# Performance work log

Hardware: AMD Instinct MI355X
Metric: run time of the kernel (lower is better)

The kernel has to match this reference:

```python
import jax, jax.numpy as jnp
import numpy as np

G = 5   # grid intervals
K = 3   # spline order
D_MODEL, D_FF = 512, 2048
B, S = 2, 2048

def make_grid():
    h = 2.0 / G
    # extended knot vector: G + 2K + 1 points spanning [-1 - K*h, 1 + K*h]
    return (jnp.arange(-K, G + K + 1, dtype=jnp.float32) * h - 1.0)

def b_splines(x, grid, k):
    # x: (N, in), grid: (G+2k+1,) -> bases: (N, in, G+k) via Cox-de Boor
    x = x[..., None]  # (N, in, 1)
    bases = ((x >= grid[:-1]) & (x < grid[1:])).astype(x.dtype)  # order-0, (N,in,G+2k)
    for j in range(1, k + 1):
        left = (x - grid[: -(j + 1)]) / (grid[j:-1] - grid[: -(j + 1)])
        right = (grid[j + 1:] - x) / (grid[j + 1:] - grid[1:-j])
        bases = left * bases[..., :-1] + right * bases[..., 1:]
    return bases

def kan_layer(x, grid, w_base, w_spline):
    # x: (N, in); w_base: (out, in); w_spline: (out, in, G+k)
    base = jax.nn.silu(x) @ w_base.T                      # residual base path
    bases = b_splines(x, grid, K)                          # (N, in, G+k)
    spline = jnp.einsum('nig,oig->no', bases, w_spline)    # per-edge spline contraction
    return base + spline

def setup_inputs() -> dict:
    key = jax.random.key(0)
    ks = jax.random.split(key, 5)
    sc1 = 1.0 / np.sqrt(D_MODEL)
    sc2 = 1.0 / np.sqrt(D_FF)
    return {
        'x': jax.random.normal(ks[0], (B, S, D_MODEL), dtype=jnp.float32),
        'grid': make_grid(),
        'w1_base': jax.random.normal(ks[1], (D_FF, D_MODEL), dtype=jnp.float32) * sc1,
        'w1_spline': jax.random.normal(ks[2], (D_FF, D_MODEL, G + K), dtype=jnp.float32) * (0.1 * sc1),
        'w2_base': jax.random.normal(ks[3], (D_MODEL, D_FF), dtype=jnp.float32) * sc2,
        'w2_spline': jax.random.normal(ks[4], (D_MODEL, D_FF, G + K), dtype=jnp.float32) * (0.1 * sc2),
    }

def reference(x, grid, w1_base, w1_spline, w2_base, w2_spline):
    b, s, d = x.shape
    xf = x.reshape(-1, d)                      # (N, d_model)
    h = kan_layer(xf, grid, w1_base, w1_spline)   # (N, d_ff)
    out = kan_layer(h, grid, w2_base, w2_spline)  # (N, d_model)
    return out.reshape(b, s, d)
```

## Files before the change

kernel.cpp:

```cpp
#include <hip/hip_runtime.h>
#include <stdint.h>


typedef __bf16 bf16x8_t __attribute__((ext_vector_type(8)));
typedef float f32x4_t __attribute__((ext_vector_type(4)));

__device__ __forceinline__ float bf2f(unsigned short u) {
    union { float f; uint32_t i; } c; c.i = ((uint32_t)u) << 16; return c.f;
}
__device__ __forceinline__ unsigned short f2bf(float f) {
    union { float f; uint32_t u; } c; c.f = f;
    uint32_t u = c.u;
    u += 0x7FFFu + ((u >> 16) & 1u);
    return (unsigned short)(u >> 16);
}
__device__ __forceinline__ bool f32world(const void* gridp) {
    return ((*(const unsigned int*)gridp) & 0xFFFFu) == 0xCCCDu;
}

__global__ __launch_bounds__(256)
void cvt4_kernel(const void* __restrict__ s0, const void* __restrict__ s1,
                 const void* __restrict__ s2, const void* __restrict__ s3,
                 unsigned short* __restrict__ dst, const void* __restrict__ gridp)
{
    const int n0 = 262144;
    const int n01 = n0 + 2097152;
    const int n012 = n01 + 262144;
    const int n = n012 + 2097152;
    int i = blockIdx.x * 256 + threadIdx.x;
    if (i >= n) return;
    const void* src; long off;
    if      (i < n0)   { src = s0; off = i; }
    else if (i < n01)  { src = s1; off = i - n0; }
    else if (i < n012) { src = s2; off = i - n01; }
    else               { src = s3; off = i - n012; }
    if (f32world(gridp)) {
        float4 v = ((const float4*)src)[off];
        ushort4 o;
        o.x = f2bf(v.x); o.y = f2bf(v.y); o.z = f2bf(v.z); o.w = f2bf(v.w);
        ((ushort4*)dst)[i] = o;
    } else {
        ((ushort4*)dst)[i] = ((const ushort4*)src)[off];
    }
}

template<int XMODE>
__global__ __launch_bounds__(256)
void act_kernel(const void* __restrict__ Xv, const void* __restrict__ gridp,
                unsigned short* __restrict__ S, unsigned short* __restrict__ BS,
                int total4)
{
    int gi = blockIdx.x * 256 + threadIdx.x;
    if (gi >= total4) return;

    const bool w32 = f32world(gridp);

    float t[12];
    if (w32) {
        const float* g = (const float*)gridp;
#pragma unroll
        for (int k = 0; k < 12; ++k) t[k] = g[k];
    } else {
        const unsigned short* g = (const unsigned short*)gridp;
#pragma unroll
        for (int k = 0; k < 12; ++k) t[k] = bf2f(g[k]);
    }
    const float rr[3] = {1.0f / (t[1] - t[0]), 1.0f / (t[2] - t[0]),
                         1.0f / (t[3] - t[0])};

    float xv[4];
    if (XMODE == 2 || (XMODE == 0 && w32)) {
        float4 v = ((const float4*)Xv)[gi];
        xv[0] = v.x; xv[1] = v.y; xv[2] = v.z; xv[3] = v.w;
    } else {
        ushort4 v = ((const ushort4*)Xv)[gi];
        xv[0] = bf2f(v.x); xv[1] = bf2f(v.y); xv[2] = bf2f(v.z); xv[3] = bf2f(v.w);
    }

    ushort4 sOut;
    unsigned short* sp = (unsigned short*)&sOut;
    int4 bsOut[4];

#pragma unroll
    for (int e = 0; e < 4; ++e) {
        float x = xv[e];
        float sg = 1.0f / (1.0f + __expf(-x));
        sp[e] = f2bf(x * sg);

        float b[11];
#pragma unroll
        for (int j = 0; j < 11; ++j)
            b[j] = (x >= t[j] && x < t[j + 1]) ? 1.0f : 0.0f;

#pragma unroll
        for (int j = 1; j <= 3; ++j) {
            float inv = rr[j - 1];
#pragma unroll
            for (int i = 0; i + j < 11; ++i) {
                float left  = (x - t[i]) * inv;
                float right = (t[i + j + 1] - x) * inv;
                b[i] = left * b[i] + right * b[i + 1];
            }
        }

        union { int4 v; unsigned short h[8]; } u;
#pragma unroll
        for (int g = 0; g < 8; ++g) u.h[g] = f2bf(b[g]);
        bsOut[e] = u.v;
    }

    ((ushort4*)S)[gi] = sOut;
    int4* bp = (int4*)&BS[(long)gi * 32];
#pragma unroll
    for (int e = 0; e < 4; ++e) bp[e] = bsOut[e];
}

template<int BM, int BN, int OUT_MODE>
__global__ __launch_bounds__(256)
void gemm_seg(const unsigned short* __restrict__ A0, int K0,
              const unsigned short* __restrict__ A1, int K1,
              const unsigned short* __restrict__ B0,
              const unsigned short* __restrict__ B1,
              void* __restrict__ Cv, int N, int crow0, int ktiles,
              const void* __restrict__ gridp)
{
    constexpr int BK = 64;
    constexpr int TM = BM / 32;
    constexpr int TN = BN / 32;

    __shared__ unsigned short As[BM * BK];
    __shared__ unsigned short Bs[BN * BK];

    const int tid  = threadIdx.x;
    const int lane = tid & 63;
    const int w    = tid >> 6;
    const int wm   = w & 1;
    const int wn   = w >> 1;

    const int gx = gridDim.x, gy = gridDim.y, gz = gridDim.z;
    int bx = blockIdx.x, by = blockIdx.y, bz = blockIdx.z;
    {
        int NB = gx * gy * gz;
        if ((NB & 7) == 0) {
            int F = bx + gx * (by + gy * bz);
            int T = (F & 7) * (NB >> 3) + (F >> 3);
            int pl = gx * gy;
            bz = T / pl;
            int r = T - bz * pl;
            by = r / gx;
            bx = r - by * gx;
        }
    }

    const int rowA0 = by * BM;
    const int colC0 = bx * BN;

    const int nkt0 = K0 / BK;
    const int nkt  = nkt0 + K1 / BK;
    const int kt0  = bz * ktiles;
    const int kt1  = (kt0 + ktiles < nkt) ? kt0 + ktiles : nkt;

    const int srow = (w << 3) + (lane >> 3);
    const int scol = (((lane & 7) ^ ((lane >> 3) & 7)) << 3);

    const int q  = lane >> 4;
    const int l7 = lane & 7;
    const int cidx0 = ((q) ^ l7) << 3;
    const int cidx1 = ((4 + q) ^ l7) << 3;

    f32x4_t acc[TM][TN];
#pragma unroll
    for (int i = 0; i < TM; ++i)
#pragma unroll
        for (int j = 0; j < TN; ++j)
            acc[i][j] = (f32x4_t){0.f, 0.f, 0.f, 0.f};

    for (int kt = kt0; kt < kt1; ++kt) {
        const unsigned short* Abase;
        const unsigned short* Bbase;
        long ld; int ko;
        if (kt < nkt0) { Abase = A0; Bbase = B0; ld = K0; ko = kt * BK; }
        else           { Abase = A1; Bbase = B1; ld = K1; ko = (kt - nkt0) * BK; }

#pragma unroll
        for (int i = 0; i < BM / 32; ++i) {
            const unsigned short* g = Abase + (long)(rowA0 + i * 32 + srow) * ld + ko + scol;
            __builtin_amdgcn_global_load_lds(
                (const __attribute__((address_space(1))) void*)g,
                (__attribute__((address_space(3))) void*)&As[(i * 32 + (w << 3)) * BK],
                16, 0, 0);
        }
#pragma unroll
        for (int i = 0; i < BN / 32; ++i) {
            const unsigned short* g = Bbase + (long)(colC0 + i * 32 + srow) * ld + ko + scol;
            __builtin_amdgcn_global_load_lds(
                (const __attribute__((address_space(1))) void*)g,
                (__attribute__((address_space(3))) void*)&Bs[(i * 32 + (w << 3)) * BK],
                16, 0, 0);
        }
        __syncthreads();

#pragma unroll
        for (int ks = 0; ks < 2; ++ks) {
            const int cidx = ks ? cidx1 : cidx0;
            bf16x8_t af[TM], bfr[TN];
#pragma unroll
            for (int tm = 0; tm < TM; ++tm)
                af[tm] = *(const bf16x8_t*)&As[(wm * (BM / 2) + tm * 16 + (lane & 15)) * BK
                                               + cidx];
#pragma unroll
            for (int tn = 0; tn < TN; ++tn)
                bfr[tn] = *(const bf16x8_t*)&Bs[(wn * (BN / 2) + tn * 16 + (lane & 15)) * BK
                                                + cidx];
#pragma unroll
            for (int tm = 0; tm < TM; ++tm)
#pragma unroll
                for (int tn = 0; tn < TN; ++tn)
                    acc[tm][tn] = __builtin_amdgcn_mfma_f32_16x16x32_bf16(
                        af[tm], bfr[tn], acc[tm][tn], 0, 0, 0);
        }
        __syncthreads();
    }

    const bool w32 = (OUT_MODE == 2) ? f32world(gridp) : false;
#pragma unroll
    for (int tm = 0; tm < TM; ++tm) {
#pragma unroll
        for (int tn = 0; tn < TN; ++tn) {
            int row0 = crow0 + rowA0 + wm * (BM / 2) + tm * 16 + (lane >> 4) * 4;
            int col  = colC0 + wn * (BN / 2) + tn * 16 + (lane & 15);
#pragma unroll
            for (int r = 0; r < 4; ++r) {
                long off = (long)(row0 + r) * N + col;
                float v = acc[tm][tn][r];
                if (OUT_MODE == 1)      unsafeAtomicAdd(&((float*)Cv)[off], v);
                else if (OUT_MODE == 0) ((unsigned short*)Cv)[off] = f2bf(v);
                else if (w32)           ((float*)Cv)[off] = v;
                else                    ((unsigned short*)Cv)[off] = f2bf(v);
            }
        }
    }
}

__global__ __launch_bounds__(256)
void accum_to_out(const float* __restrict__ acc, void* __restrict__ out,
                  int n4, const void* __restrict__ gridp)
{
    int i = blockIdx.x * 256 + threadIdx.x;
    if (i >= n4) return;
    float4 v = ((const float4*)acc)[i];
    if (f32world(gridp)) {
        ((float4*)out)[i] = v;
    } else {
        ushort4 o;
        o.x = f2bf(v.x); o.y = f2bf(v.y); o.z = f2bf(v.z); o.w = f2bf(v.w);
        ((ushort4*)out)[i] = o;
    }
}

extern "C" void kernel_launch(void* const* d_in, const int* in_sizes, int n_in,
                              void* d_out, int out_size, void* d_ws, size_t ws_size,
                              hipStream_t stream)
{
    const void* x   = d_in[0];
    const void* grd = d_in[1];
    const void* w1b = d_in[2];
    const void* w1s = d_in[3];
    const void* w2b = d_in[4];
    const void* w2s = d_in[5];

    const int NTOK = 4096, D1 = 512, D2 = 2048;
    const size_t MiB = 1024 * 1024;
    char* ws = (char*)d_ws;

    if (ws_size >= 144 * MiB) {
        unsigned short* wcat   = (unsigned short*)ws;
        unsigned short* w1b_bf = (unsigned short*)(ws);
        unsigned short* w1s_bf = (unsigned short*)(ws + 2  * MiB);
        unsigned short* w2b_bf = (unsigned short*)(ws + 18 * MiB);
        unsigned short* w2s_bf = (unsigned short*)(ws + 20 * MiB);
        unsigned short* S1     = (unsigned short*)(ws + 36 * MiB);
        unsigned short* BS1    = (unsigned short*)(ws + 40 * MiB);
        unsigned short* H      = (unsigned short*)(ws + 72 * MiB);
        unsigned short* S2     = (unsigned short*)(ws + 88 * MiB);
        float*          C2     = (float*)(ws + 104 * MiB);
        unsigned short* BS2    = (unsigned short*)(ws + 112 * MiB);

        int CT;
        if      (ws_size >= 240 * MiB) CT = 4096;
        else if (ws_size >= 176 * MiB) CT = 2048;
        else                           CT = 1024;

        cvt4_kernel<<<(4718592 + 255) / 256, 256, 0, stream>>>(w1b, w1s, w2b, w2s, wcat, grd);

        act_kernel<0><<<(NTOK * D1 / 4 + 255) / 256, 256, 0, stream>>>(
            x, grd, S1, BS1, NTOK * D1 / 4);
        {
            dim3 g(D2 / 128, NTOK / 128, 1);
            gemm_seg<128, 128, 0><<<g, 256, 0, stream>>>(
                S1, D1, BS1, D1 * 8, w1b_bf, w1s_bf, (void*)H, D2, 0, 72, grd);
        }

        hipMemsetAsync(C2, 0, (size_t)NTOK * D1 * 4, stream);
        const int SPLIT2 = 32768 / CT;
        const int KT2 = 288 / SPLIT2;
        int nch = NTOK / CT;
        for (int c = 0; c < nch; ++c) {
            long tokOff = (long)c * CT;
            act_kernel<1><<<(CT * D2 / 4 + 255) / 256, 256, 0, stream>>>(
                (const void*)(H + tokOff * D2), grd, S2, BS2, CT * D2 / 4);
            dim3 g(D1 / 128, CT / 128, SPLIT2);
            gemm_seg<128, 128, 1><<<g, 256, 0, stream>>>(
                S2, D2, BS2, D2 * 8, w2b_bf, w2s_bf,
                (void*)C2, D1, (int)tokOff, KT2, grd);
        }

        accum_to_out<<<(NTOK * D1 / 4 + 255) / 256, 256, 0, stream>>>(
            C2, d_out, NTOK * D1 / 4, grd);
    } else {
        unsigned short* w1b_bf = (unsigned short*)(ws);
        unsigned short* w1s_bf = (unsigned short*)(ws + 2  * MiB);
        unsigned short* w2b_bf = (unsigned short*)(ws + 18 * MiB);
        unsigned short* w2s_bf = (unsigned short*)(ws + 20 * MiB);
        unsigned short* H      = (unsigned short*)(ws + 36 * MiB);
        unsigned short* S1     = (unsigned short*)(ws + 52 * MiB);
        unsigned short* BS1    = (unsigned short*)(ws + 56 * MiB);
        unsigned short* S2     = (unsigned short*)(ws + 52 * MiB);
        unsigned short* BS2    = (unsigned short*)(ws + 68 * MiB);

        int CT;
        if      (ws_size >= 100 * MiB) CT = 1024;
        else                           CT = 256;

        cvt4_kernel<<<(4718592 + 255) / 256, 256, 0, stream>>>(
            w1b, w1s, w2b, w2s, (unsigned short*)ws, grd);

        {
            act_kernel<0><<<(NTOK * D1 / 4 + 255) / 256, 256, 0, stream>>>(
                x, grd, S1, BS1, NTOK * D1 / 4);
            dim3 g(D2 / 128, NTOK / 128, 1);
            gemm_seg<128, 128, 0><<<g, 256, 0, stream>>>(
                S1, D1, BS1, D1 * 8, w1b_bf, w1s_bf, (void*)H, D2, 0, 72, grd);
        }
        int nch = NTOK / CT;
        for (int c = 0; c < nch; ++c) {
            long tokOff = (long)c * CT;
            act_kernel<1><<<(CT * D2 / 4 + 255) / 256, 256, 0, stream>>>(
                (const void*)(H + tokOff * D2), grd, S2 + tokOff * D2, BS2, CT * D2 / 4);
            dim3 g(D1 / 128, CT / 64, 1);
            gemm_seg<64, 128, 2><<<g, 256, 0, stream>>>(
                S2 + tokOff * D2, D2, BS2, D2 * 8, w2b_bf, w2s_bf,
                d_out, D1, (int)tokOff, 288, grd);
        }
    }
}
```

Baseline: 393.6 us.

## Split-K the first KAN GEMM into two partial buffers and fold memset into activation

The first-layer GEMM now runs with two K-splits along grid z. Each split writes its own bf16 partial H buffer at an offset of zstride, which roughly doubles the block count for that GEMM. The second-layer activation kernel adds a mode that reads both partials and sums them before computing SiLU and the B-spline bases. The separate memset of the fp32 accumulator is folded into the first activation chunk. In exchange, H traffic roughly doubles, each partial is rounded to bf16 before the sum, and the fast path now needs a larger workspace threshold.

```diff
diff --git a/kernel.cpp b/kernel.cpp
--- a/kernel.cpp
+++ b/kernel.cpp
@@ -48,10 +48,12 @@
 __global__ __launch_bounds__(256)
 void act_kernel(const void* __restrict__ Xv, const void* __restrict__ gridp,
                 unsigned short* __restrict__ S, unsigned short* __restrict__ BS,
-                int total4)
+                int total4, long pair_off, float* __restrict__ zbuf, int zn4)
 {
     int gi = blockIdx.x * 256 + threadIdx.x;
     if (gi >= total4) return;
+
+    if (zbuf && gi < zn4) ((float4*)zbuf)[gi] = (float4){0.f, 0.f, 0.f, 0.f};
 
     const bool w32 = f32world(gridp);
 
@@ -69,9 +71,14 @@
                          1.0f / (t[3] - t[0])};
 
     float xv[4];
-    if (XMODE == 2 || (XMODE == 0 && w32)) {
+    if (XMODE == 0 && w32) {
         float4 v = ((const float4*)Xv)[gi];
         xv[0] = v.x; xv[1] = v.y; xv[2] = v.z; xv[3] = v.w;
+    } else if (XMODE == 3) {
+        ushort4 a = ((const ushort4*)Xv)[gi];
+        ushort4 b = ((const ushort4*)((const unsigned short*)Xv + pair_off))[gi];
+        xv[0] = bf2f(a.x) + bf2f(b.x); xv[1] = bf2f(a.y) + bf2f(b.y);
+        xv[2] = bf2f(a.z) + bf2f(b.z); xv[3] = bf2f(a.w) + bf2f(b.w);
     } else {
         ushort4 v = ((const ushort4*)Xv)[gi];
         xv[0] = bf2f(v.x); xv[1] = bf2f(v.y); xv[2] = bf2f(v.z); xv[3] = bf2f(v.w);
@@ -122,7 +129,7 @@
               const unsigned short* __restrict__ B0,
               const unsigned short* __restrict__ B1,
               void* __restrict__ Cv, int N, int crow0, int ktiles,
-              const void* __restrict__ gridp)
+              long zstride, const void* __restrict__ gridp)
 {
     constexpr int BK = 64;
     constexpr int TM = BM / 32;
@@ -223,6 +230,7 @@
     }
 
     const bool w32 = (OUT_MODE == 2) ? f32world(gridp) : false;
+    const long zoff = (OUT_MODE == 0) ? (long)bz * zstride : 0;
 #pragma unroll
     for (int tm = 0; tm < TM; ++tm) {
 #pragma unroll
@@ -234,7 +242,7 @@
                 long off = (long)(row0 + r) * N + col;
                 float v = acc[tm][tn][r];
                 if (OUT_MODE == 1)      unsafeAtomicAdd(&((float*)Cv)[off], v);
-                else if (OUT_MODE == 0) ((unsigned short*)Cv)[off] = f2bf(v);
+                else if (OUT_MODE == 0) ((unsigned short*)Cv)[off + zoff] = f2bf(v);
                 else if (w32)           ((float*)Cv)[off] = v;
                 else                    ((unsigned short*)Cv)[off] = f2bf(v);
             }
@@ -273,7 +281,7 @@
     const size_t MiB = 1024 * 1024;
     char* ws = (char*)d_ws;
 
-    if (ws_size >= 144 * MiB) {
+    if (ws_size >= 160 * MiB) {
         unsigned short* wcat   = (unsigned short*)ws;
         unsigned short* w1b_bf = (unsigned short*)(ws);
         unsigned short* w1s_bf = (unsigned short*)(ws + 2  * MiB);
@@ -281,38 +289,41 @@
         unsigned short* w2s_bf = (unsigned short*)(ws + 20 * MiB);
         unsigned short* S1     = (unsigned short*)(ws + 36 * MiB);
         unsigned short* BS1    = (unsigned short*)(ws + 40 * MiB);
-        unsigned short* H      = (unsigned short*)(ws + 72 * MiB);
-        unsigned short* S2     = (unsigned short*)(ws + 88 * MiB);
-        float*          C2     = (float*)(ws + 104 * MiB);
-        unsigned short* BS2    = (unsigned short*)(ws + 112 * MiB);
+        unsigned short* Ha     = (unsigned short*)(ws + 72 * MiB);
+        unsigned short* Hb     = (unsigned short*)(ws + 88 * MiB);
+        unsigned short* S2     = (unsigned short*)(ws + 104 * MiB);
+        float*          C2     = (float*)(ws + 120 * MiB);
+        unsigned short* BS2    = (unsigned short*)(ws + 128 * MiB);
 
         int CT;
-        if      (ws_size >= 240 * MiB) CT = 4096;
-        else if (ws_size >= 176 * MiB) CT = 2048;
+        if      (ws_size >= 256 * MiB) CT = 4096;
+        else if (ws_size >= 192 * MiB) CT = 2048;
         else                           CT = 1024;
 
         cvt4_kernel<<<(4718592 + 255) / 256, 256, 0, stream>>>(w1b, w1s, w2b, w2s, wcat, grd);
 
         act_kernel<0><<<(NTOK * D1 / 4 + 255) / 256, 256, 0, stream>>>(
-            x, grd, S1, BS1, NTOK * D1 / 4);
+            x, grd, S1, BS1, NTOK * D1 / 4, 0, nullptr, 0);
         {
-            dim3 g(D2 / 128, NTOK / 128, 1);
+            dim3 g(D2 / 128, NTOK / 128, 2);
             gemm_seg<128, 128, 0><<<g, 256, 0, stream>>>(
-                S1, D1, BS1, D1 * 8, w1b_bf, w1s_bf, (void*)H, D2, 0, 72, grd);
-        }
-
-        hipMemsetAsync(C2, 0, (size_t)NTOK * D1 * 4, stream);
+                S1, D1, BS1, D1 * 8, w1b_bf, w1s_bf, (void*)Ha, D2, 0, 36,
+                (long)NTOK * D2, grd);
+        }
+
         const int SPLIT2 = 32768 / CT;
         const int KT2 = 288 / SPLIT2;
+        const long HOFF = (long)NTOK * D2;
         int nch = NTOK / CT;
         for (int c = 0; c < nch; ++c) {
             long tokOff = (long)c * CT;
-            act_kernel<1><<<(CT * D2 / 4 + 255) / 256, 256, 0, stream>>>(
-                (const void*)(H + tokOff * D2), grd, S2, BS2, CT * D2 / 4);
+            act_kernel<3><<<(CT * D2 / 4 + 255) / 256, 256, 0, stream>>>(
+                (const void*)(Ha + tokOff * D2), grd, S2, BS2, CT * D2 / 4,
+                HOFF, (c == 0) ? (float*)C2 : nullptr, NTOK * D1 / 4);
             dim3 g(D1 / 128, CT / 128, SPLIT2);
             gemm_seg<128, 128, 1><<<g, 256, 0, stream>>>(
                 S2, D2, BS2, D2 * 8, w2b_bf, w2s_bf,
-                (void*)C2, D1, (int)tokOff, KT2, grd);
+                (void*)C2, D1, (int)tokOff, KT2, 0, grd);
         }
 
         accum_to_out<<<(NTOK * D1 / 4 + 255) / 256, 256, 0, stream>>>(
@@ -337,20 +348,21 @@
 
         {
             act_kernel<0><<<(NTOK * D1 / 4 + 255) / 256, 256, 0, stream>>>(
-                x, grd, S1, BS1, NTOK * D1 / 4);
+                x, grd, S1, BS1, NTOK * D1 / 4, 0, nullptr, 0);
             dim3 g(D2 / 128, NTOK / 128, 1);
             gemm_seg<128, 128, 0><<<g, 256, 0, stream>>>(
-                S1, D1, BS1, D1 * 8, w1b_bf, w1s_bf, (void*)H, D2, 0, 72, grd);
+                S1, D1, BS1, D1 * 8, w1b_bf, w1s_bf, (void*)H, D2, 0, 72, 0, grd);
         }
         int nch = NTOK / CT;
         for (int c = 0; c < nch; ++c) {
             long tokOff = (long)c * CT;
             act_kernel<1><<<(CT * D2 / 4 + 255) / 256, 256, 0, stream>>>(
-                (const void*)(H + tokOff * D2), grd, S2 + tokOff * D2, BS2, CT * D2 / 4);
+                (const void*)(H + tokOff * D2), grd, S2 + tokOff * D2, BS2,
+                CT * D2 / 4, 0, nullptr, 0);
             dim3 g(D1 / 128, CT / 64, 1);
             gemm_seg<64, 128, 2><<<g, 256, 0, stream>>>(
                 S2 + tokOff * D2, D2, BS2, D2 * 8, w2b_bf, w2s_bf,
-                d_out, D1, (int)tokOff, 288, grd);
-        }
-    }
-}
+                d_out, D1, (int)tokOff, 288, 0, grd);
+        }
+    }
+}
```

Measured after the change: 391.2 us. No clear change (-0.6%).
